# Performance work log

Measured on AMD Instinct MI355X. Metric: run time of the kernel, lower is better.

The kernel has to match this reference:

```python
import jax, jax.numpy as jnp
import numpy as np
import math

D_MODEL, H, D_FF = 1024, 16, 4096
B, S = 4, 2048
EPS = 1e-6

def layer_norm(x, alpha, beta):
    # Faithful to torch: x.std uses Bessel correction (ddof=1), eps added to std.
    mean = jnp.mean(x, axis=-1, keepdims=True)
    std = jnp.std(x, axis=-1, keepdims=True, ddof=1)
    return alpha * (x - mean) / (std + EPS) + beta

def setup_inputs() -> dict:
    key = jax.random.key(0)
    ks = jax.random.split(key, 8)
    sc = 0.02
    return {
        "x": jax.random.normal(ks[0], (B, S, D_MODEL), jnp.float32),
        "mask": jnp.ones((B, 1, 1, S), jnp.int32),
        "wq": jax.random.normal(ks[1], (D_MODEL, D_MODEL), jnp.float32) * sc,
        "wk": jax.random.normal(ks[2], (D_MODEL, D_MODEL), jnp.float32) * sc,
        "wv": jax.random.normal(ks[3], (D_MODEL, D_MODEL), jnp.float32) * sc,
        "wo": jax.random.normal(ks[4], (D_MODEL, D_MODEL), jnp.float32) * sc,
        "w1": jax.random.normal(ks[5], (D_MODEL, D_FF), jnp.float32) * sc,
        "b1": jnp.zeros((D_FF,), jnp.float32),
        "w2": jax.random.normal(ks[6], (D_FF, D_MODEL), jnp.float32) * sc,
        "b2": jnp.zeros((D_MODEL,), jnp.float32),
        "ln1_a": jnp.ones((D_MODEL,), jnp.float32),
        "ln1_b": jnp.zeros((D_MODEL,), jnp.float32),
        "ln2_a": jnp.ones((D_MODEL,), jnp.float32),
        "ln2_b": jnp.zeros((D_MODEL,), jnp.float32),
    }

def mha(xn, mask, wq, wk, wv, wo):
    b, s, d = xn.shape
    d_k = d // H
    q = (xn @ wq).reshape(b, s, H, d_k).transpose(0, 2, 1, 3)  # [B,H,S,dk]
    k = (xn @ wk).reshape(b, s, H, d_k).transpose(0, 2, 1, 3)
    v = (xn @ wv).reshape(b, s, H, d_k).transpose(0, 2, 1, 3)
    scores = jnp.einsum('bhqd,bhkd->bhqk', q, k) / math.sqrt(d_k)
    scores = jnp.where(mask == 0, -1e9, scores)
    attn = jax.nn.softmax(scores, axis=-1)
    out = jnp.einsum('bhqk,bhkd->bhqd', attn, v)
    out = out.transpose(0, 2, 1, 3).reshape(b, s, d)
    return out @ wo

def reference(x, mask, wq, wk, wv, wo, w1, b1, w2, b2, ln1_a, ln1_b, ln2_a, ln2_b):
    # Pre-LN residual 1: self-attention (dropout=0 / eval mode -> identity)
    xn = layer_norm(x, ln1_a, ln1_b)
    x = x + mha(xn, mask, wq, wk, wv, wo)
    # Pre-LN residual 2: FFN
    xn = layer_norm(x, ln2_a, ln2_b)
    ff = jax.nn.relu(xn @ w1 + b1) @ w2 + b2
    return x + ff
```

## Files before the change

kernel.cpp:

```cpp
#include <hip/hip_runtime.h>
#include <hip/hip_bf16.h>

typedef __bf16 bf16x8 __attribute__((ext_vector_type(8)));
typedef __bf16 bf16x4 __attribute__((ext_vector_type(4)));
typedef float  f32x4  __attribute__((ext_vector_type(4)));

#define MFMA(a, b, c) __builtin_amdgcn_mfma_f32_16x16x32_bf16((a), (b), (c), 0, 0, 0)

#define GLOAD16(gp, lp) __builtin_amdgcn_global_load_lds(                      \
    (const __attribute__((address_space(1))) void*)(gp),                       \
    (__attribute__((address_space(3))) void*)(lp), 16, 0, 0)

__device__ inline unsigned int pkbf(float a, float b) {
    __bf16 x = (__bf16)a, y = (__bf16)b;
    return (unsigned int)*(unsigned short*)&x |
           ((unsigned int)*(unsigned short*)&y << 16);
}

__global__ __launch_bounds__(256) void transpose_cvt(
    const float* __restrict__ src, __bf16* __restrict__ dst, int Kd, int Nd)
{
    __shared__ float tile[32][33];
    const int k0 = blockIdx.y * 32, n0 = blockIdx.x * 32;
    const int t = threadIdx.x;
    const int r = t >> 5, c = t & 31;
#pragma unroll
    for (int i = 0; i < 4; ++i)
        tile[r + i * 8][c] = src[(long)(k0 + r + i * 8) * Nd + n0 + c];
    __syncthreads();
#pragma unroll
    for (int i = 0; i < 4; ++i)
        dst[(long)(n0 + r + i * 8) * Kd + k0 + c] = (__bf16)tile[c][r + i * 8];
}

__global__ __launch_bounds__(256) void transpose_v(
    const __bf16* __restrict__ V, __bf16* __restrict__ Vt)
{
    __shared__ __bf16 tile[32][33];
    const int bh = blockIdx.z;
    const int s0 = blockIdx.x * 32, d0 = blockIdx.y * 32;
    const int t = threadIdx.x, r = t >> 5, c = t & 31;
    const __bf16* Vp = V + (long)bh * 2048 * 64;
    __bf16* Tp = Vt + (long)bh * 64 * 2048;
#pragma unroll
    for (int i = 0; i < 4; ++i)
        tile[r + i * 8][c] = Vp[(long)(s0 + r + i * 8) * 64 + d0 + c];
    __syncthreads();
#pragma unroll
    for (int i = 0; i < 4; ++i)
        Tp[(long)(d0 + r + i * 8) * 2048 + s0 + c] = tile[c][r + i * 8];
}

__global__ __launch_bounds__(256) void ln_kernel(
    const float* __restrict__ in, const float* __restrict__ ga,
    const float* __restrict__ gb, __bf16* __restrict__ out)
{
    const int row = blockIdx.x;
    const int t = threadIdx.x;
    const float4 xv = *(const float4*)(in + (long)row * 1024 + t * 4);
    float s  = xv.x + xv.y + xv.z + xv.w;
    float sq = xv.x * xv.x + xv.y * xv.y + xv.z * xv.z + xv.w * xv.w;
#pragma unroll
    for (int off = 32; off; off >>= 1) {
        s  += __shfl_xor(s, off);
        sq += __shfl_xor(sq, off);
    }
    __shared__ float red[8];
    const int w = t >> 6;
    if ((t & 63) == 0) { red[w * 2] = s; red[w * 2 + 1] = sq; }
    __syncthreads();
    s  = red[0] + red[2] + red[4] + red[6];
    sq = red[1] + red[3] + red[5] + red[7];
    const float mean = s * (1.0f / 1024.0f);
    const float var  = fmaxf((sq - s * mean) * (1.0f / 1023.0f), 0.0f);
    const float dinv = 1.0f / (sqrtf(var) + 1e-6f);
    const float4 av = *(const float4*)(ga + t * 4);
    const float4 bv = *(const float4*)(gb + t * 4);
    bf16x4 o;
    o[0] = (__bf16)((xv.x - mean) * dinv * av.x + bv.x);
    o[1] = (__bf16)((xv.y - mean) * dinv * av.y + bv.y);
    o[2] = (__bf16)((xv.z - mean) * dinv * av.z + bv.z);
    o[3] = (__bf16)((xv.w - mean) * dinv * av.w + bv.w);
    *(bf16x4*)(out + (long)row * 1024 + t * 4) = o;
}

template <int MODE>
__global__ __launch_bounds__(256) void gemm_bt(
    const __bf16* __restrict__ A, const __bf16* __restrict__ Bt,
    int M, int N, int K,
    const float* __restrict__ bias, const float* resid,
    float* outf, __bf16* __restrict__ outb,
    __bf16* __restrict__ qb, __bf16* __restrict__ kb, __bf16* __restrict__ vb)
{
    __shared__ __align__(16) __bf16 Alds[128 * 32];
    __shared__ __align__(16) __bf16 Blds[128 * 32];

    const int t = threadIdx.x;
    const int lane = t & 63, w = t >> 6;
    const int wr = w >> 1, wc = w & 1;
    const int g = lane >> 4, l15 = lane & 15;
    const int bm = blockIdx.y * 128, bn = blockIdx.x * 128;

    const int cr = t >> 2;
    const int cc = (t & 3) * 8;
    const __bf16* Ag  = A  + (long)(bm + cr) * K + cc;
    const __bf16* Ag2 = Ag + (long)64 * K;
    const __bf16* Bg  = Bt + (long)(bn + cr) * K + cc;
    const __bf16* Bg2 = Bg + (long)64 * K;
    char* Alp = (char*)Alds + t * 16;
    char* Blp = (char*)Blds + t * 16;

    f32x4 acc[4][4] = {};
    const int nk = K / 32;

    for (int kt = 0; kt < nk; ++kt) {
        const long ko = (long)kt * 32;
        __syncthreads();
        GLOAD16(Ag + ko,  Alp);
        GLOAD16(Ag2 + ko, Alp + 4096);
        GLOAD16(Bg + ko,  Blp);
        GLOAD16(Bg2 + ko, Blp + 4096);
        __syncthreads();
        bf16x8 af[4], bfr[4];
#pragma unroll
        for (int mi = 0; mi < 4; ++mi)
            af[mi] = *(const bf16x8*)(Alds + (wr * 64 + mi * 16 + l15) * 32 + g * 8);
#pragma unroll
        for (int ni = 0; ni < 4; ++ni)
            bfr[ni] = *(const bf16x8*)(Blds + (wc * 64 + ni * 16 + l15) * 32 + g * 8);
#pragma unroll
        for (int mi = 0; mi < 4; ++mi)
#pragma unroll
            for (int ni = 0; ni < 4; ++ni)
                acc[mi][ni] = MFMA(af[mi], bfr[ni], acc[mi][ni]);
    }

#pragma unroll
    for (int mi = 0; mi < 4; ++mi) {
#pragma unroll
        for (int ni = 0; ni < 4; ++ni) {
#pragma unroll
            for (int r = 0; r < 4; ++r) {
                const int gr = bm + wr * 64 + mi * 16 + g * 4 + r;
                const int gc = bn + wc * 64 + ni * 16 + l15;
                const float vacc = acc[mi][ni][r];
                if constexpr (MODE == 0) {
                    const int bufi = gc >> 10;
                    const int hd = gc & 1023;
                    const int h = hd >> 6, d = hd & 63;
                    const int b = gr >> 11, sx = gr & 2047;
                    __bf16* dst = (bufi == 0) ? qb : ((bufi == 1) ? kb : vb);
                    dst[((long)((b * 16 + h) * 2048 + sx)) * 64 + d] = (__bf16)vacc;
                } else if constexpr (MODE == 1) {
                    const long idx = (long)gr * N + gc;
                    outf[idx] = vacc + resid[idx];
                } else if constexpr (MODE == 2) {
                    const float y = fmaxf(vacc + bias[gc], 0.0f);
                    outb[(long)gr * N + gc] = (__bf16)y;
                } else {
                    const long idx = (long)gr * N + gc;
                    outf[idx] = vacc + bias[gc] + resid[idx];
                }
            }
        }
    }
}

__global__ __launch_bounds__(256, 2) void attn_kernel(
    const __bf16* __restrict__ Q, const __bf16* __restrict__ Kk,
    const __bf16* __restrict__ Vt, const int* __restrict__ mask,
    __bf16* __restrict__ O)
{
    __shared__ __align__(16) char Klds[8192];
    __shared__ __align__(16) char Vlds[8192];
    __shared__ int mlds[64];

    const int t = threadIdx.x;
    const int lane = t & 63, w = t >> 6;
    const int g = lane >> 4, l15 = lane & 15;
    const int bh = blockIdx.x >> 4;
    const int qt = blockIdx.x & 15;
    const int b = bh >> 4, h = bh & 15;
    const int q0 = qt * 128 + w * 32;

    const __bf16* Qp = Q  + (long)bh * 2048 * 64;
    const __bf16* Kp = Kk + (long)bh * 2048 * 64;
    const __bf16* Vp = Vt + (long)bh * 64 * 2048;
    const int* mp = mask + b * 2048;

    bf16x8 qreg[2][2];
#pragma unroll
    for (int qf = 0; qf < 2; ++qf)
#pragma unroll
        for (int kh = 0; kh < 2; ++kh)
            qreg[qf][kh] = *(const bf16x8*)(Qp + (long)(q0 + qf * 16 + l15) * 64 + kh * 32 + g * 8);

    float m_run[2] = {-1e30f, -1e30f}, l_run[2] = {0.0f, 0.0f};
    f32x4 ot[2][4] = {};

    const int sr0 = t >> 3;
    const int sce = (t & 7) * 8;
    const int swz0 = sr0 * 128 + (((t & 7) * 16) ^ ((sr0 & 7) << 4));
    const int swz1 = swz0 + 32 * 128;

    bf16x8 kr0 = *(const bf16x8*)(Kp + (long)sr0 * 64 + sce);
    bf16x8 kr1 = *(const bf16x8*)(Kp + (long)(sr0 + 32) * 64 + sce);
    bf16x8 vr0 = *(const bf16x8*)(Vp + (long)sr0 * 2048 + sce);
    bf16x8 vr1 = *(const bf16x8*)(Vp + (long)(sr0 + 32) * 2048 + sce);
    int mr = (t < 64) ? mp[t] : 0;

    for (int kc = 0; kc < 32; ++kc) {
        __syncthreads();
        *(bf16x8*)(Klds + swz0) = kr0;
        *(bf16x8*)(Klds + swz1) = kr1;
        *(bf16x8*)(Vlds + swz0) = vr0;
        *(bf16x8*)(Vlds + swz1) = vr1;
        if (t < 64) mlds[t] = mr;
        __syncthreads();
        if (kc < 31) {
            const int kv0 = (kc + 1) * 64;
            kr0 = *(const bf16x8*)(Kp + (long)(kv0 + sr0) * 64 + sce);
            kr1 = *(const bf16x8*)(Kp + (long)(kv0 + sr0 + 32) * 64 + sce);
            vr0 = *(const bf16x8*)(Vp + (long)sr0 * 2048 + kv0 + sce);
            vr1 = *(const bf16x8*)(Vp + (long)(sr0 + 32) * 2048 + kv0 + sce);
            if (t < 64) mr = mp[kv0 + t];
        }

        bf16x8 kf[4][2];
#pragma unroll
        for (int f = 0; f < 4; ++f)
#pragma unroll
            for (int dh = 0; dh < 2; ++dh)
                kf[f][dh] = *(const bf16x8*)(Klds + (f * 16 + l15) * 128 +
                                             (((dh * 64 + g * 16)) ^ ((l15 & 7) << 4)));
        f32x4 sf[2][4] = {};
        __builtin_amdgcn_s_setprio(1);
#pragma unroll
        for (int qf = 0; qf < 2; ++qf)
#pragma unroll
            for (int f = 0; f < 4; ++f) {
                sf[qf][f] = MFMA(kf[f][0], qreg[qf][0], sf[qf][f]);
                sf[qf][f] = MFMA(kf[f][1], qreg[qf][1], sf[qf][f]);
            }
        __builtin_amdgcn_s_setprio(0);

        int mvv[16];
#pragma unroll
        for (int f = 0; f < 4; ++f) {
            const int4 mq = *(const int4*)&mlds[f * 16 + g * 4];
            mvv[f * 4 + 0] = mq.x; mvv[f * 4 + 1] = mq.y;
            mvv[f * 4 + 2] = mq.z; mvv[f * 4 + 3] = mq.w;
        }

        bf16x8 av[4][2];
#pragma unroll
        for (int df = 0; df < 4; ++df)
#pragma unroll
            for (int hh = 0; hh < 2; ++hh)
                av[df][hh] = *(const bf16x8*)(Vlds + (df * 16 + l15) * 128 +
                                              (((hh * 64 + g * 16)) ^ ((l15 & 7) << 4)));

#pragma unroll
        for (int qf = 0; qf < 2; ++qf) {
            float s[16], p[16];
            float mx = -1e30f;
#pragma unroll
            for (int i = 0; i < 16; ++i) {
                float xs = sf[qf][i >> 2][i & 3] * 0.125f;
                if (mvv[i] == 0) xs = -1e9f;
                s[i] = xs;
                mx = fmaxf(mx, xs);
            }
            mx = fmaxf(mx, __shfl_xor(mx, 16));
            mx = fmaxf(mx, __shfl_xor(mx, 32));
            const float m_new = fmaxf(m_run[qf], mx);
            const float alpha = __expf(m_run[qf] - m_new);
            float ps = 0.0f;
#pragma unroll
            for (int i = 0; i < 16; ++i) { p[i] = __expf(s[i] - m_new); ps += p[i]; }
            ps += __shfl_xor(ps, 16);
            ps += __shfl_xor(ps, 32);
            l_run[qf] = l_run[qf] * alpha + ps;
            m_run[qf] = m_new;
#pragma unroll
            for (int df = 0; df < 4; ++df)
#pragma unroll
                for (int r = 0; r < 4; ++r) ot[qf][df][r] *= alpha;

#pragma unroll
            for (int hh = 0; hh < 2; ++hh) {
                unsigned int u0 = pkbf(p[hh * 8 + 0], p[hh * 8 + 1]);
                unsigned int u1 = pkbf(p[hh * 8 + 2], p[hh * 8 + 3]);
                unsigned int u2 = pkbf(p[hh * 8 + 4], p[hh * 8 + 5]);
                unsigned int u3 = pkbf(p[hh * 8 + 6], p[hh * 8 + 7]);
                const unsigned int a0 = __shfl_xor(u0, 16), a1 = __shfl_xor(u1, 16);
                const unsigned int b0 = __shfl_xor(u2, 16), b1 = __shfl_xor(u3, 16);
                const bool ge = ((g & 1) == 0);
                const unsigned int E0 = ge ? u0 : a0, E1 = ge ? u1 : a1;
                const unsigned int E2 = ge ? a0 : u0, E3 = ge ? a1 : u1;
                const unsigned int F0 = ge ? u2 : b0, F1 = ge ? u3 : b1;
                const unsigned int F2 = ge ? b0 : u2, F3 = ge ? b1 : u3;
                const unsigned int S0 = (g < 2) ? F0 : E0, S1 = (g < 2) ? F1 : E1;
                const unsigned int S2 = (g < 2) ? F2 : E2, S3 = (g < 2) ? F3 : E3;
                const unsigned int R0 = __shfl_xor(S0, 32), R1 = __shfl_xor(S1, 32);
                const unsigned int R2 = __shfl_xor(S2, 32), R3 = __shfl_xor(S3, 32);
                unsigned int P0 = (g == 0) ? E0 : (g == 3) ? F0 : R0;
                unsigned int P1 = (g == 0) ? E1 : (g == 3) ? F1 : R1;
                unsigned int P2 = (g == 0) ? E2 : (g == 3) ? F2 : R2;
                unsigned int P3 = (g == 0) ? E3 : (g == 3) ? F3 : R3;
                unsigned int pu[4] = {P0, P1, P2, P3};
                bf16x8 pf = *(bf16x8*)pu;
                __builtin_amdgcn_s_setprio(1);
#pragma unroll
                for (int df = 0; df < 4; ++df)
                    ot[qf][df] = MFMA(av[df][hh], pf, ot[qf][df]);
                __builtin_amdgcn_s_setprio(0);
            }
        }
    }

#pragma unroll
    for (int qf = 0; qf < 2; ++qf) {
        const float inv = 1.0f / l_run[qf];
        const int q = q0 + qf * 16 + l15;
        __bf16* orow = O + (long)(b * 2048 + q) * 1024 + h * 64;
#pragma unroll
        for (int df = 0; df < 4; ++df)
#pragma unroll
            for (int rp = 0; rp < 2; ++rp) {
                const int d = df * 16 + g * 4 + rp * 2;
                *(unsigned int*)(orow + d) =
                    pkbf(ot[qf][df][rp * 2] * inv, ot[qf][df][rp * 2 + 1] * inv);
            }
    }
}

extern "C" void kernel_launch(void* const* d_in, const int* in_sizes, int n_in,
                              void* d_out, int out_size, void* d_ws, size_t ws_size,
                              hipStream_t stream)
{
    const float* x    = (const float*)d_in[0];
    const int*   mask = (const int*)  d_in[1];
    const float* wq   = (const float*)d_in[2];
    const float* wk   = (const float*)d_in[3];
    const float* wv   = (const float*)d_in[4];
    const float* wo   = (const float*)d_in[5];
    const float* w1   = (const float*)d_in[6];
    const float* b1   = (const float*)d_in[7];
    const float* w2   = (const float*)d_in[8];
    const float* b2   = (const float*)d_in[9];
    const float* l1a  = (const float*)d_in[10];
    const float* l1b  = (const float*)d_in[11];
    const float* l2a  = (const float*)d_in[12];
    const float* l2b  = (const float*)d_in[13];
    float* out = (float*)d_out;

    char* ws = (char*)d_ws;
    __bf16* wqkvT = (__bf16*)(ws);
    __bf16* woT   = (__bf16*)(ws + 6291456);
    __bf16* w1T   = (__bf16*)(ws + 8388608);
    __bf16* w2T   = (__bf16*)(ws + 16777216);
    __bf16* xn    = (__bf16*)(ws + 25165824);
    __bf16* Vtb   = (__bf16*)(ws + 25165824);
    __bf16* Qb    = (__bf16*)(ws + 41943040);
    __bf16* Kb    = (__bf16*)(ws + 58720256);
    __bf16* Vb    = (__bf16*)(ws + 75497472);
    __bf16* attO  = (__bf16*)(ws + 92274688);
    __bf16* ffh   = (__bf16*)(ws + 41943040);

    transpose_cvt<<<dim3(32, 32),  256, 0, stream>>>(wq, wqkvT,               1024, 1024);
    transpose_cvt<<<dim3(32, 32),  256, 0, stream>>>(wk, wqkvT + 1024 * 1024, 1024, 1024);
    transpose_cvt<<<dim3(32, 32),  256, 0, stream>>>(wv, wqkvT + 2048 * 1024, 1024, 1024);
    transpose_cvt<<<dim3(32, 32),  256, 0, stream>>>(wo, woT,                 1024, 1024);
    transpose_cvt<<<dim3(128, 32), 256, 0, stream>>>(w1, w1T,                 1024, 4096);
    transpose_cvt<<<dim3(32, 128), 256, 0, stream>>>(w2, w2T,                 4096, 1024);

    ln_kernel<<<8192, 256, 0, stream>>>(x, l1a, l1b, xn);
    gemm_bt<0><<<dim3(24, 64), 256, 0, stream>>>(xn, wqkvT, 8192, 3072, 1024,
                                                 nullptr, nullptr, nullptr, nullptr, Qb, Kb, Vb);
    transpose_v<<<dim3(64, 2, 64), 256, 0, stream>>>(Vb, Vtb);
    attn_kernel<<<1024, 256, 0, stream>>>(Qb, Kb, Vtb, mask, attO);
    gemm_bt<1><<<dim3(8, 64), 256, 0, stream>>>(attO, woT, 8192, 1024, 1024,
                                                nullptr, x, out, nullptr, nullptr, nullptr, nullptr);
    ln_kernel<<<8192, 256, 0, stream>>>(out, l2a, l2b, xn);
    gemm_bt<2><<<dim3(32, 64), 256, 0, stream>>>(xn, w1T, 8192, 4096, 1024,
                                                 b1, nullptr, nullptr, ffh, nullptr, nullptr, nullptr);
    gemm_bt<3><<<dim3(8, 64), 256, 0, stream>>>(ffh, w2T, 8192, 1024, 4096,
                                                b2, out, out, nullptr, nullptr, nullptr, nullptr);
    (void)in_sizes; (void)n_in; (void)out_size; (void)ws_size;
}
```

Measured before the change: 532.4 us.

## Remap GEMM tiles, use lazy exp2 softmax, and drop P shuffles in attention

The GEMM blocks get an XCD-aware tile remapping so neighbouring tiles land on the same chiplet. The attention kernel folds the 1/sqrt(dk) scale and log2(e) into a single exp2 fma, and only rescales the accumulator when the running max grows by more than a threshold. It also replaces the cross-lane shuffle that rearranged P with a V fragment loaded in a permuted order from LDS, so P can be fed to the MFMA directly. The launch bound is raised to 4 waves per SIMD, which tightens register pressure and risks spilling. The tile remap assumes the grid size is divisible by 8, and the lazy rescale relies on the fp32 range absorbing an exponent offset of up to 2^8.

Result: slower. 746.1 us (+40.1%).

```diff
diff --git a/kernel.cpp b/kernel.cpp
--- a/kernel.cpp
+++ b/kernel.cpp
@@ -99,7 +99,12 @@
     const int lane = t & 63, w = t >> 6;
     const int wr = w >> 1, wc = w & 1;
     const int g = lane >> 4, l15 = lane & 15;
-    const int bm = blockIdx.y * 128, bn = blockIdx.x * 128;
+
+    const int nwg = gridDim.x * gridDim.y;
+    const int hwid = blockIdx.y * gridDim.x + blockIdx.x;
+    const int wid = (hwid & 7) * (nwg >> 3) + (hwid >> 3);
+    const int bm = (wid / gridDim.x) * 128;
+    const int bn = (wid % gridDim.x) * 128;
 
     const int cr = t >> 2;
     const int cc = (t & 3) * 8;
@@ -166,7 +171,7 @@
     }
 }
 
-__global__ __launch_bounds__(256, 2) void attn_kernel(
+__global__ __launch_bounds__(256, 4) void attn_kernel(
     const __bf16* __restrict__ Q, const __bf16* __restrict__ Kk,
     const __bf16* __restrict__ Vt, const int* __restrict__ mask,
     __bf16* __restrict__ O)
@@ -195,7 +200,8 @@
         for (int kh = 0; kh < 2; ++kh)
             qreg[qf][kh] = *(const bf16x8*)(Qp + (long)(q0 + qf * 16 + l15) * 64 + kh * 32 + g * 8);
 
-    float m_run[2] = {-1e30f, -1e30f}, l_run[2] = {0.0f, 0.0f};
+    const float Csc = 0.18033688011112042f;
+    float m2_run[2] = {-1e30f, -1e30f}, l_run[2] = {0.0f, 0.0f};
     f32x4 ot[2][4] = {};
 
     const int sr0 = t >> 3;
@@ -232,7 +238,7 @@
 #pragma unroll
             for (int dh = 0; dh < 2; ++dh)
                 kf[f][dh] = *(const bf16x8*)(Klds + (f * 16 + l15) * 128 +
-                                             (((dh * 64 + g * 16)) ^ ((l15 & 7) << 4)));
+                                             ((dh * 64 + g * 16) ^ ((l15 & 7) << 4)));
         f32x4 sf[2][4] = {};
         __builtin_amdgcn_s_setprio(1);
 #pragma unroll
@@ -254,61 +260,61 @@
 
         bf16x8 av[4][2];
 #pragma unroll
-        for (int df = 0; df < 4; ++df)
-#pragma unroll
-            for (int hh = 0; hh < 2; ++hh)
-                av[df][hh] = *(const bf16x8*)(Vlds + (df * 16 + l15) * 128 +
-                                              (((hh * 64 + g * 16)) ^ ((l15 & 7) << 4)));
+        for (int df = 0; df < 4; ++df) {
+            const int row = (df * 16 + l15) * 128;
+            const int sx = (l15 & 7) << 4;
+#pragma unroll
+            for (int hh = 0; hh < 2; ++hh) {
+                const bf16x4 lo = *(const bf16x4*)(Vlds + row + ((hh * 64 + g * 8) ^ sx));
+                const bf16x4 hi = *(const bf16x4*)(Vlds + row + ((hh * 64 + 32 + g * 8) ^ sx));
+                bf16x8 a;
+                a[0] = lo[0]; a[1] = lo[1]; a[2] = lo[2]; a[3] = lo[3];
+                a[4] = hi[0]; a[5] = hi[1]; a[6] = hi[2]; a[7] = hi[3];
+                av[df][hh] = a;
+            }
+        }
 
 #pragma unroll
         for (int qf = 0; qf < 2; ++qf) {
-            float s[16], p[16];
+            float s[16];
             float mx = -1e30f;
 #pragma unroll
             for (int i = 0; i < 16; ++i) {
-                float xs = sf[qf][i >> 2][i & 3] * 0.125f;
+                float xs = sf[qf][i >> 2][i & 3];
                 if (mvv[i] == 0) xs = -1e9f;
                 s[i] = xs;
                 mx = fmaxf(mx, xs);
             }
             mx = fmaxf(mx, __shfl_xor(mx, 16));
             mx = fmaxf(mx, __shfl_xor(mx, 32));
-            const float m_new = fmaxf(m_run[qf], mx);
-            const float alpha = __expf(m_run[qf] - m_new);
-            float ps = 0.0f;
-#pragma unroll
-            for (int i = 0; i < 16; ++i) { p[i] = __expf(s[i] - m_new); ps += p[i]; }
+            const float m2 = mx * Csc;
+            if (!__all(m2 - m2_run[qf] <= 8.0f)) {
+                const float m2n = fmaxf(m2_run[qf], m2);
+                const float alpha = __builtin_amdgcn_exp2f(m2_run[qf] - m2n);
+                l_run[qf] *= alpha;
+#pragma unroll
+                for (int df = 0; df < 4; ++df)
+#pragma unroll
+                    for (int r = 0; r < 4; ++r) ot[qf][df][r] *= alpha;
+                m2_run[qf] = m2n;
+            }
+            const float nm2 = -m2_run[qf];
+            float p[16], ps = 0.0f;
+#pragma unroll
+            for (int i = 0; i < 16; ++i) {
+                p[i] = __builtin_amdgcn_exp2f(__builtin_fmaf(s[i], Csc, nm2));
+                ps += p[i];
+            }
             ps += __shfl_xor(ps, 16);
             ps += __shfl_xor(ps, 32);
-            l_run[qf] = l_run[qf] * alpha + ps;
-            m_run[qf] = m_new;
-#pragma unroll
-            for (int df = 0; df < 4; ++df)
-#pragma unroll
-                for (int r = 0; r < 4; ++r) ot[qf][df][r] *= alpha;
+            l_run[qf] += ps;
 
 #pragma unroll
             for (int hh = 0; hh < 2; ++hh) {
-                unsigned int u0 = pkbf(p[hh * 8 + 0], p[hh * 8 + 1]);
-                unsigned int u1 = pkbf(p[hh * 8 + 2], p[hh * 8 + 3]);
-                unsigned int u2 = pkbf(p[hh * 8 + 4], p[hh * 8 + 5]);
-                unsigned int u3 = pkbf(p[hh * 8 + 6], p[hh * 8 + 7]);
-                const unsigned int a0 = __shfl_xor(u0, 16), a1 = __shfl_xor(u1, 16);
-                const unsigned int b0 = __shfl_xor(u2, 16), b1 = __shfl_xor(u3, 16);
-                const bool ge = ((g & 1) == 0);
-                const unsigned int E0 = ge ? u0 : a0, E1 = ge ? u1 : a1;
-                const unsigned int E2 = ge ? a0 : u0, E3 = ge ? a1 : u1;
-                const unsigned int F0 = ge ? u2 : b0, F1 = ge ? u3 : b1;
-                const unsigned int F2 = ge ? b0 : u2, F3 = ge ? b1 : u3;
-                const unsigned int S0 = (g < 2) ? F0 : E0, S1 = (g < 2) ? F1 : E1;
-                const unsigned int S2 = (g < 2) ? F2 : E2, S3 = (g < 2) ? F3 : E3;
-                const unsigned int R0 = __shfl_xor(S0, 32), R1 = __shfl_xor(S1, 32);
-                const unsigned int R2 = __shfl_xor(S2, 32), R3 = __shfl_xor(S3, 32);
-                unsigned int P0 = (g == 0) ? E0 : (g == 3) ? F0 : R0;
-                unsigned int P1 = (g == 0) ? E1 : (g == 3) ? F1 : R1;
-                unsigned int P2 = (g == 0) ? E2 : (g == 3) ? F2 : R2;
-                unsigned int P3 = (g == 0) ? E3 : (g == 3) ? F3 : R3;
-                unsigned int pu[4] = {P0, P1, P2, P3};
+                unsigned int pu[4] = {pkbf(p[hh * 8 + 0], p[hh * 8 + 1]),
+                                      pkbf(p[hh * 8 + 2], p[hh * 8 + 3]),
+                                      pkbf(p[hh * 8 + 4], p[hh * 8 + 5]),
+                                      pkbf(p[hh * 8 + 6], p[hh * 8 + 7])};
                 bf16x8 pf = *(bf16x8*)pu;
                 __builtin_amdgcn_s_setprio(1);
 #pragma unroll
```
